# Kernel optimization log

Hardware: AMD Instinct MI355X
Metric: run time of the kernel (lower is better)

The kernel has to match this reference:

```python
import jax, jax.numpy as jnp
import numpy as np

B, S, D = 1, 512, 2048
H, KVH, HD = 16, 16, 128          # heads, kv heads, head_dim = D // H
E, K, I = 64, 6, 1408             # routed experts, top_k, moe intermediate
NSH = 2
ISH = NSH * I                     # shared expert intermediate
EPS = 1e-6
THETA = 10000.0
SCALE = HD ** -0.5


def setup_inputs() -> dict:
    key = jax.random.key(0)
    ks = jax.random.split(key, 12)
    s = 0.02
    rn = lambda k, shape: s * jax.random.normal(k, shape, dtype=jnp.float32)
    return {
        "positions": jnp.arange(B * S, dtype=jnp.int32).reshape(B, S),
        "hidden_states": jax.random.normal(ks[0], (B, S, D), dtype=jnp.float32),
        "residual": jax.random.normal(ks[1], (B, S, D), dtype=jnp.float32),
        "ln1_w": jnp.ones((D,), jnp.float32),
        "ln2_w": jnp.ones((D,), jnp.float32),
        "wqkv": rn(ks[2], ((H + 2 * KVH) * HD, D)),
        "wo": rn(ks[3], (D, H * HD)),
        "gate_w": rn(ks[4], (E, D)),
        "w1": rn(ks[5], (E, 2 * I, D)),   # packed gate_up per expert
        "w2": rn(ks[6], (E, D, I)),       # down per expert
        "sw1": rn(ks[7], (2 * ISH, D)),   # shared expert gate_up
        "sw2": rn(ks[8], (D, ISH)),       # shared expert down
    }


def _rmsnorm(x, w):
    var = jnp.mean(x * x, axis=-1, keepdims=True)
    return x * jax.lax.rsqrt(var + EPS) * w


def _rope(x, pos):
    # x: [B, S, n_heads, HD], neox style (rotate halves), full rotary dim
    half = HD // 2
    inv_freq = 1.0 / (THETA ** (jnp.arange(half, dtype=jnp.float32) * 2.0 / HD))
    ang = pos.astype(jnp.float32)[..., None] * inv_freq        # [B, S, half]
    cos = jnp.cos(ang)[:, :, None, :]
    sin = jnp.sin(ang)[:, :, None, :]
    x1, x2 = jnp.split(x, 2, axis=-1)
    return jnp.concatenate([x1 * cos - x2 * sin, x2 * cos + x1 * sin], axis=-1)


def _swiglu(x, w_gate_up, w_down):
    gu = x @ w_gate_up.T
    g, u = jnp.split(gu, 2, axis=-1)
    return (jax.nn.silu(g) * u) @ w_down.T


def reference(positions, hidden_states, residual, ln1_w, ln2_w, wqkv, wo,
              gate_w, w1, w2, sw1, sw2):
    # --- input_layernorm with fused residual add (vLLM RMSNorm semantics) ---
    x = hidden_states + residual
    residual = x
    h = _rmsnorm(x, ln1_w)

    # --- attention: qkv proj, RoPE, causal attention (prefill), o proj ---
    qkv = h @ wqkv.T                                           # [B, S, (H+2KVH)*HD]
    q, k, v = jnp.split(qkv, [H * HD, (H + KVH) * HD], axis=-1)
    q = q.reshape(B, S, H, HD)
    k = k.reshape(B, S, KVH, HD)
    v = v.reshape(B, S, KVH, HD)
    q = _rope(q, positions)
    k = _rope(k, positions)
    scores = jnp.einsum("bqhd,bkhd->bhqk", q, k) * SCALE
    causal = jnp.tril(jnp.ones((S, S), dtype=bool))
    scores = jnp.where(causal, scores, -jnp.inf)
    attn = jax.nn.softmax(scores, axis=-1)
    ctx = jnp.einsum("bhqk,bkhd->bqhd", attn, v).reshape(B, S, H * HD)
    h = ctx @ wo.T

    # --- post_attention_layernorm with fused residual add ---
    x = h + residual
    residual = x
    h = _rmsnorm(x, ln2_w)

    # --- MoE: shared expert + softmax gate + top-k dispatch ---
    xt = h.reshape(B * S, D)                                   # [T, D]
    T = B * S
    shared = _swiglu(xt, sw1, sw2)                             # [T, D]
    logits = xt @ gate_w.T                                     # [T, E]
    probs = jax.nn.softmax(logits.astype(jnp.float32), axis=-1)
    topw, topi = jax.lax.top_k(probs, K)                       # [T, K]
    # norm_topk_prob = False -> no renormalization
    combine = jnp.zeros((T, E), jnp.float32).at[
        jnp.arange(T)[:, None], topi].add(topw)                # [T, E]

    def expert_step(acc, ew):
        w1e, w2e, ce = ew                                      # [2I,D], [D,I], [T]
        out = _swiglu(xt, w1e, w2e)                            # [T, D]
        return acc + ce[:, None] * out, None

    moe_out, _ = jax.lax.scan(expert_step, jnp.zeros_like(xt),
                              (w1, w2, combine.T))
    out = (moe_out + shared).reshape(B, S, D)
    return out, residual
```

## Files before the change

### kernel.cpp

```cpp
#include <hip/hip_runtime.h>
#include <hip/hip_bf16.h>


typedef __attribute__((ext_vector_type(4))) float  f32x4;
typedef __attribute__((ext_vector_type(8))) short  short8;
typedef __attribute__((ext_vector_type(8))) unsigned short ushort8;

#define SS    512
#define DD    2048
#define NH    16
#define HDIM  128
#define NQKV  6144
#define NEXP  64
#define TOPK  6
#define IEXP  1408
#define ISHE  2816
#define MAXTILE 128
#define ATT_SCALE 0.08838834764831845f

__device__ __forceinline__ float u2f(unsigned short u) {
  return __uint_as_float(((unsigned int)u) << 16);
}
__device__ __forceinline__ unsigned short f2u(float f) {
  __hip_bfloat16 h = __float2bfloat16(f);
  return *reinterpret_cast<unsigned short*>(&h);
}
__device__ __forceinline__ ushort8 cvt8(f32x4 a, f32x4 b) {
  ushort8 r;
  r[0]=f2u(a[0]); r[1]=f2u(a[1]); r[2]=f2u(a[2]); r[3]=f2u(a[3]);
  r[4]=f2u(b[0]); r[5]=f2u(b[1]); r[6]=f2u(b[2]); r[7]=f2u(b[3]);
  return r;
}

typedef __attribute__((address_space(3))) unsigned int lds_uint;
typedef const __attribute__((address_space(1))) unsigned int ga_uint;
__device__ __forceinline__ void gll16(const void* g, void* l) {
  __builtin_amdgcn_global_load_lds((ga_uint*)g, (lds_uint*)l, 16, 0, 0);
}

__global__ __launch_bounds__(256) void cvtw_k(
    const float* __restrict__ wqkv, const float* __restrict__ wo,
    const float* __restrict__ sw1, const float* __restrict__ sw2,
    unsigned short* __restrict__ wqkv_bf, unsigned short* __restrict__ wo_bf,
    unsigned short* __restrict__ sw1_bf, unsigned short* __restrict__ sw2_bf)
{
  long long i = ((long long)blockIdx.x * 256 + threadIdx.x) * 8;
  const long long S1 = (long long)NQKV * DD;
  const long long S2 = S1 + (long long)DD * DD;
  const long long S3 = S2 + (long long)2 * ISHE * DD;
  const float* src; unsigned short* dst; long long j;
  if (i < S1)      { src = wqkv; dst = wqkv_bf; j = i; }
  else if (i < S2) { src = wo;   dst = wo_bf;   j = i - S1; }
  else if (i < S3) { src = sw1;  dst = sw1_bf;  j = i - S2; }
  else             { src = sw2;  dst = sw2_bf;  j = i - S3; }
  f32x4 a = *(const f32x4*)(src + j);
  f32x4 b = *(const f32x4*)(src + j + 4);
  *(ushort8*)(dst + j) = cvt8(a, b);
}

__global__ __launch_bounds__(256) void addnorm1_k(
    const float* __restrict__ hid, const float* __restrict__ res,
    const float* __restrict__ w, float* __restrict__ x1,
    unsigned short* __restrict__ h1)
{
  int t = blockIdx.x, tid = threadIdx.x;
  long long base = (long long)t * DD + tid * 8;
  float x[8]; float ss = 0.f;
#pragma unroll
  for (int i = 0; i < 8; i++) {
    x[i] = hid[base + i] + res[base + i];
    ss += x[i] * x[i]; x1[base + i] = x[i];
  }
#pragma unroll
  for (int o = 1; o < 64; o <<= 1) ss += __shfl_xor(ss, o);
  __shared__ float r4[4];
  if ((tid & 63) == 0) r4[tid >> 6] = ss;
  __syncthreads();
  ss = r4[0] + r4[1] + r4[2] + r4[3];
  float rr = rsqrtf(ss * (1.f / DD) + 1e-6f);
#pragma unroll
  for (int i = 0; i < 8; i++) h1[base + i] = f2u(x[i] * rr * w[tid * 8 + i]);
}

__global__ __launch_bounds__(256) void addnorm2_k(
    const unsigned short* __restrict__ attn, const float* __restrict__ x1,
    const float* __restrict__ w, float* __restrict__ resid_out,
    unsigned short* __restrict__ h3)
{
  int t = blockIdx.x, tid = threadIdx.x;
  long long base = (long long)t * DD + tid * 8;
  ushort8 va = *(const ushort8*)(attn + base);
  float x[8]; float ss = 0.f;
#pragma unroll
  for (int i = 0; i < 8; i++) {
    x[i] = u2f(va[i]) + x1[base + i]; ss += x[i] * x[i];
    resid_out[base + i] = x[i];
  }
#pragma unroll
  for (int o = 1; o < 64; o <<= 1) ss += __shfl_xor(ss, o);
  __shared__ float r4[4];
  if ((tid & 63) == 0) r4[tid >> 6] = ss;
  __syncthreads();
  ss = r4[0] + r4[1] + r4[2] + r4[3];
  float rr = rsqrtf(ss * (1.f / DD) + 1e-6f);
#pragma unroll
  for (int i = 0; i < 8; i++) h3[base + i] = f2u(x[i] * rr * w[tid * 8 + i]);
}

__global__ __launch_bounds__(256) void gemm_bb(
    const unsigned short* __restrict__ A, const unsigned short* __restrict__ W,
    unsigned short* __restrict__ C, int Nh, int K, int lda)
{
  __shared__ __align__(16) unsigned short As[2][64][64];
  __shared__ __align__(16) unsigned short Bs[2][64][64];

  int m0 = blockIdx.y * 64;
  int n0 = blockIdx.x * 64;
  int tid = threadIdx.x, lane = tid & 63, w = tid >> 6;

  const unsigned short* asrc[2];
  const unsigned short* bsrc[2];
#pragma unroll
  for (int i = 0; i < 2; i++) {
    int c = w + i * 4;
    int r = c * 8 + (lane >> 3);
    int col = ((lane & 7) ^ (lane >> 3)) << 3;
    asrc[i] = A + (long long)(m0 + r) * lda + col;
    bsrc[i] = W + (long long)(n0 + r) * K + col;
  }

  int wm = (w >> 1) * 32, wn = (w & 1) * 32;
  int l15 = lane & 15, hi = lane >> 4;
  int key = l15 & 7;

  f32x4 acc[2][2] = {};

#define BSTAGE(buf, k0)                                                  \
  do {                                                                   \
    gll16((const char*)asrc[0] + (k0) * 2, &As[buf][w * 8][0]);          \
    gll16((const char*)asrc[1] + (k0) * 2, &As[buf][(w + 4) * 8][0]);    \
    gll16((const char*)bsrc[0] + (k0) * 2, &Bs[buf][w * 8][0]);          \
    gll16((const char*)bsrc[1] + (k0) * 2, &Bs[buf][(w + 4) * 8][0]);    \
  } while (0)

  BSTAGE(0, 0);
  int buf = 0;
  for (int k0 = 0; k0 < K; k0 += 64, buf ^= 1) {
    __syncthreads();
    if (k0 + 64 < K) BSTAGE(buf ^ 1, k0 + 64);
#pragma unroll
    for (int kk = 0; kk < 2; kk++) {
      short8 fa[2], fb[2];
#pragma unroll
      for (int f = 0; f < 2; f++) {
        fa[f] = *(const short8*)&As[buf][wm + f * 16 + l15][(((kk << 2) + hi) ^ key) << 3];
        fb[f] = *(const short8*)&Bs[buf][wn + f * 16 + l15][(((kk << 2) + hi) ^ key) << 3];
      }
#pragma unroll
      for (int fm = 0; fm < 2; fm++)
#pragma unroll
        for (int fn = 0; fn < 2; fn++)
          acc[fm][fn] = __builtin_amdgcn_mfma_f32_16x16x32_bf16(fa[fm], fb[fn], acc[fm][fn], 0, 0, 0);
    }
  }
#undef BSTAGE

  int r0q = hi * 4;
#pragma unroll
  for (int fm = 0; fm < 2; fm++) {
#pragma unroll
    for (int j = 0; j < 4; j++) {
      int m = m0 + wm + fm * 16 + r0q + j;
      unsigned short* Cp = C + (long long)m * Nh + n0 + wn;
#pragma unroll
      for (int fn = 0; fn < 2; fn++)
        Cp[fn * 16 + l15] = f2u(acc[fm][fn][j]);
    }
  }
}

template<int STAGE>
__global__ __launch_bounds__(256) void moe_k(
    const unsigned short* __restrict__ h3,
    const unsigned short* __restrict__ act_e_in, const unsigned short* __restrict__ act_sh_in,
    const float* __restrict__ w1, const unsigned short* __restrict__ sw1_bf,
    const float* __restrict__ w2, const unsigned short* __restrict__ sw2_bf,
    unsigned short* __restrict__ act_e_out, unsigned short* __restrict__ act_sh_out,
    unsigned short* __restrict__ out_e, unsigned short* __restrict__ shared_o,
    const int* __restrict__ e_cnt, const int* __restrict__ e_off,
    const int* __restrict__ tok_list, const float* __restrict__ wslot,
    const int* __restrict__ tile_tab, const int* __restrict__ ntiles)
{
  constexpr bool SILU = (STAGE == 0);
  __shared__ __align__(16) unsigned short As[64][72];
  __shared__ __align__(16) unsigned short Bg[64][72];
  __shared__ __align__(16) unsigned short Bu[SILU ? 64 : 1][72];

  int yr = blockIdx.y;
  int y = (yr < 8) ? yr : 8 + ((yr - 8) & 7) * 15 + ((yr - 8) >> 3);
  if (y >= *ntiles) return;
  int tt = tile_tab[y];
  int e = tt >> 8;
  int m0 = (tt & 255) * 64;
  bool sh = (e == NEXP);
  int cnt  = sh ? SS : e_cnt[e];
  int roff = sh ? 0 : e_off[e];
  int n0 = blockIdx.x * 64;

  int Nh, K, lda;
  const float* Wb32 = nullptr;
  const unsigned short* Wb16 = nullptr;
  const unsigned short* Abase;
  unsigned short* Cb;
  if (STAGE == 0) {
    K = DD; lda = DD; Abase = h3;
    if (sh) { Nh = ISHE; Wb16 = sw1_bf; Cb = act_sh_out; }
    else    { Nh = IEXP; Wb32 = w1 + (long long)e * 2 * IEXP * DD; Cb = act_e_out; }
    if (n0 >= Nh) return;
  } else {
    Nh = DD;
    if (sh) { K = ISHE; lda = ISHE; Abase = act_sh_in; Wb16 = sw2_bf; Cb = shared_o; }
    else    { K = IEXP; lda = IEXP; Abase = act_e_in;
              Wb32 = w2 + (long long)e * DD * IEXP; Cb = out_e; }
  }

  int tid = threadIdx.x;
  int sr  = tid >> 2;
  int sce = (tid & 3) * 16;

  int am = m0 + sr; if (am >= cnt) am = cnt - 1;
  int arow;
  if (STAGE == 0) arow = sh ? am : tok_list[roff + am];
  else            arow = sh ? am : roff + am;
  const unsigned short* ap = Abase + (long long)arow * lda + sce;
  const float*          gp32 = Wb32 ? (Wb32 + (long long)(n0 + sr) * K + sce) : nullptr;
  const float*          up32 = (Wb32 && SILU) ? (Wb32 + (long long)(Nh + n0 + sr) * K + sce) : nullptr;
  const unsigned short* gp16 = Wb16 ? (Wb16 + (long long)(n0 + sr) * K + sce) : nullptr;
  const unsigned short* up16 = (Wb16 && SILU) ? (Wb16 + (long long)(Nh + n0 + sr) * K + sce) : nullptr;

  int lane = tid & 63, wid = tid >> 6;
  int wm = (wid >> 1) * 32, wn = (wid & 1) * 32;
  int l15 = lane & 15, hi = lane >> 4;

  f32x4 acc[2][2] = {};
  f32x4 accU[2][2] = {};
  ushort8 raA0, raA1, raB0, raB1;
  f32x4 rgA[4], ruA[4], rgB[4], ruB[4];
  union BC { f32x4 f; ushort8 s; };

#define MLOAD(k, r0, r1, g, u)                                     \
  do {                                                             \
    r0 = *(const ushort8*)(ap + (k));                              \
    r1 = *(const ushort8*)(ap + (k) + 8);                          \
    if (sh) {                                                      \
      g[0] = *(const f32x4*)(gp16 + (k));                          \
      g[1] = *(const f32x4*)(gp16 + (k) + 8);                      \
      if (SILU) {                                                  \
        u[0] = *(const f32x4*)(up16 + (k));                        \
        u[1] = *(const f32x4*)(up16 + (k) + 8);                    \
      }                                                            \
    } else {                                                       \
      _Pragma("unroll")                                            \
      for (int i_ = 0; i_ < 4; i_++) g[i_] = *(const f32x4*)(gp32 + (k) + 4 * i_); \
      if (SILU) {                                                  \
        _Pragma("unroll")                                          \
        for (int i_ = 0; i_ < 4; i_++) u[i_] = *(const f32x4*)(up32 + (k) + 4 * i_); \
      }                                                            \
    }                                                              \
  } while (0)

#define MSTORE(r0, r1, g, u)                                       \
  do {                                                             \
    *(ushort8*)&As[sr][sce]     = r0;                              \
    *(ushort8*)&As[sr][sce + 8] = r1;                              \
    if (sh) {                                                      \
      BC b0, b1; b0.f = g[0]; b1.f = g[1];                         \
      *(ushort8*)&Bg[sr][sce]     = b0.s;                          \
      *(ushort8*)&Bg[sr][sce + 8] = b1.s;                          \
      if (SILU) {                                                  \
        BC c0, c1; c0.f = u[0]; c1.f = u[1];                       \
        *(ushort8*)&Bu[sr][sce]     = c0.s;                        \
        *(ushort8*)&Bu[sr][sce + 8] = c1.s;                        \
      }                                                            \
    } else {                                                       \
      *(ushort8*)&Bg[sr][sce]     = cvt8(g[0], g[1]);              \
      *(ushort8*)&Bg[sr][sce + 8] = cvt8(g[2], g[3]);              \
      if (SILU) {                                                  \
        *(ushort8*)&Bu[sr][sce]     = cvt8(u[0], u[1]);            \
        *(ushort8*)&Bu[sr][sce + 8] = cvt8(u[2], u[3]);            \
      }                                                            \
    }                                                              \
  } while (0)

#define MMFMA                                                      \
  do {                                                             \
    _Pragma("unroll")                                              \
    for (int kk = 0; kk < 2; kk++) {                               \
      int kc = kk * 32 + hi * 8;                                   \
      short8 fa[2], fg[2];                                         \
      _Pragma("unroll")                                            \
      for (int f = 0; f < 2; f++) {                                \
        fa[f] = *(const short8*)&As[wm + f * 16 + l15][kc];        \
        fg[f] = *(const short8*)&Bg[wn + f * 16 + l15][kc];        \
      }                                                            \
      _Pragma("unroll")                                            \
      for (int fm = 0; fm < 2; fm++)                               \
        _Pragma("unroll")                                          \
        for (int fn = 0; fn < 2; fn++)                             \
          acc[fm][fn] = __builtin_amdgcn_mfma_f32_16x16x32_bf16(fa[fm], fg[fn], acc[fm][fn], 0, 0, 0); \
      if (SILU) {                                                  \
        short8 fu[2];                                              \
        _Pragma("unroll")                                          \
        for (int f = 0; f < 2; f++) fu[f] = *(const short8*)&Bu[wn + f * 16 + l15][kc]; \
        _Pragma("unroll")                                          \
        for (int fm = 0; fm < 2; fm++)                             \
          _Pragma("unroll")                                        \
          for (int fn = 0; fn < 2; fn++)                           \
            accU[fm][fn] = __builtin_amdgcn_mfma_f32_16x16x32_bf16(fa[fm], fu[fn], accU[fm][fn], 0, 0, 0); \
      }                                                            \
    }                                                              \
  } while (0)

  MLOAD(0,  raA0, raA1, rgA, ruA);
  MLOAD(64, raB0, raB1, rgB, ruB);
  for (int k0 = 0; k0 < K; k0 += 128) {
    __syncthreads();
    MSTORE(raA0, raA1, rgA, ruA);
    __syncthreads();
    if (k0 + 128 < K) MLOAD(k0 + 128, raA0, raA1, rgA, ruA);
    MMFMA;
    __syncthreads();
    MSTORE(raB0, raB1, rgB, ruB);
    __syncthreads();
    if (k0 + 192 < K) MLOAD(k0 + 192, raB0, raB1, rgB, ruB);
    MMFMA;
  }
#undef MLOAD
#undef MSTORE
#undef MMFMA

  int r0q = hi * 4;
#pragma unroll
  for (int fm = 0; fm < 2; fm++) {
#pragma unroll
    for (int j = 0; j < 4; j++) {
      int m = m0 + wm + fm * 16 + r0q + j;
      if (m >= cnt) continue;
      long long crow = sh ? m : (roff + m);
      float scale = (STAGE == 1 && !sh) ? wslot[crow] : 1.f;
      unsigned short* Cp = Cb + crow * (long long)Nh + n0 + wn;
#pragma unroll
      for (int fn = 0; fn < 2; fn++) {
        float v;
        if (SILU) {
          float g = acc[fm][fn][j], u = accU[fm][fn][j];
          v = (g / (1.f + __expf(-g))) * u;
        } else v = acc[fm][fn][j];
        Cp[fn * 16 + l15] = f2u(v * scale);
      }
    }
  }
}

__global__ __launch_bounds__(256) void rope_k(
    const int* __restrict__ pos, const unsigned short* __restrict__ qkv,
    unsigned short* __restrict__ qr, unsigned short* __restrict__ kr)
{
  int t = blockIdx.x, tid = threadIdx.x;
  __shared__ float cs[64], sn[64];
  if (tid < 64) {
    float inv = __expf(-((float)(2 * tid) / 128.f) * logf(10000.f));
    float ang = (float)pos[t] * inv;
    cs[tid] = cosf(ang); sn[tid] = sinf(ang);
  }
  __syncthreads();
  const unsigned short* row = qkv + (long long)t * NQKV;
  for (int idx = tid; idx < NH * 64; idx += 256) {
    int hh = idx >> 6, i = idx & 63;
    long long o = ((long long)hh * SS + t) * HDIM;
    float x1 = u2f(row[hh*128 + i]), x2 = u2f(row[hh*128 + i + 64]);
    qr[o + i]      = f2u(x1 * cs[i] - x2 * sn[i]);
    qr[o + i + 64] = f2u(x2 * cs[i] + x1 * sn[i]);
    float y1 = u2f(row[2048 + hh*128 + i]), y2 = u2f(row[2048 + hh*128 + i + 64]);
    kr[o + i]      = f2u(y1 * cs[i] - y2 * sn[i]);
    kr[o + i + 64] = f2u(y2 * cs[i] + y1 * sn[i]);
  }
}

__global__ __launch_bounds__(128) void attn_k(
    const unsigned short* __restrict__ qr, const unsigned short* __restrict__ kr,
    const unsigned short* __restrict__ qkv, unsigned short* __restrict__ ctx)
{
  int h = blockIdx.x, qt = blockIdx.y, q0 = qt * 32;
  int tid = threadIdx.x, lane = tid & 63, w = tid >> 6;
  int l15 = lane & 15, hi = lane >> 4;

  __shared__ unsigned short Vt[128][72];
  __shared__ unsigned short Pl[2][16][72];

  short8 qf[4];
  const unsigned short* Qb = qr + ((long long)h * SS + q0 + w * 16 + l15) * HDIM + hi * 8;
#pragma unroll
  for (int kf = 0; kf < 4; kf++) qf[kf] = *(const short8*)(Qb + kf * 32);

  f32x4 o[8] = {};
  float m_run[4] = {-1e30f, -1e30f, -1e30f, -1e30f};
  float l_run[4] = {};
  int myq = w * 16 + hi * 4;

  int T = (q0 + 31) >> 6;
  int qoff = q0 - 64 * T;
  for (int kt = 0; kt <= T; kt++) {
    int kbase = kt * 64;
    __syncthreads();
    {
      int r = lane, d0 = w * 64;
      const unsigned short* Vp = qkv + (long long)(kbase + r) * NQKV + 4096 + h * HDIM + d0;
#pragma unroll
      for (int c = 0; c < 8; c++) {
        ushort8 v = *(const ushort8*)(Vp + c * 8);
#pragma unroll
        for (int i = 0; i < 8; i++) Vt[d0 + c * 8 + i][r] = v[i];
      }
    }
    f32x4 s[4] = {};
    const unsigned short* Kb = kr + ((long long)h * SS + kbase) * HDIM + hi * 8;
#pragma unroll
    for (int nf = 0; nf < 4; nf++) {
      const unsigned short* Kp = Kb + (long long)(nf * 16 + l15) * HDIM;
#pragma unroll
      for (int kf = 0; kf < 4; kf++) {
        short8 kf8 = *(const short8*)(Kp + kf * 32);
        s[nf] = __builtin_amdgcn_mfma_f32_16x16x32_bf16(qf[kf], kf8, s[nf], 0, 0, 0);
      }
    }
    bool last = (kt == T);
#pragma unroll
    for (int nf = 0; nf < 4; nf++) {
      int keyl = nf * 16 + l15;
#pragma unroll
      for (int j = 0; j < 4; j++) {
        float sv = s[nf][j] * ATT_SCALE;
        if (last && keyl > qoff + myq + j) sv = -1e30f;
        s[nf][j] = sv;
      }
    }
    float corr[4], mnew[4];
#pragma unroll
    for (int j = 0; j < 4; j++) {
      float mv = fmaxf(fmaxf(s[0][j], s[1][j]), fmaxf(s[2][j], s[3][j]));
#pragma unroll
      for (int ox = 1; ox < 16; ox <<= 1) mv = fmaxf(mv, __shfl_xor(mv, ox));
      mnew[j] = fmaxf(m_run[j], mv);
      corr[j] = __expf(m_run[j] - mnew[j]);
      m_run[j] = mnew[j];
    }
#pragma unroll
    for (int nf8 = 0; nf8 < 8; nf8++)
#pragma unroll
      for (int j = 0; j < 4; j++) o[nf8][j] *= corr[j];
    float rs[4] = {};
#pragma unroll
    for (int nf = 0; nf < 4; nf++) {
#pragma unroll
      for (int j = 0; j < 4; j++) {
        float pv = __expf(s[nf][j] - mnew[j]);
        rs[j] += pv;
        Pl[w][hi * 4 + j][nf * 16 + l15] = f2u(pv);
      }
    }
#pragma unroll
    for (int j = 0; j < 4; j++) {
      float sv = rs[j];
#pragma unroll
      for (int ox = 1; ox < 16; ox <<= 1) sv += __shfl_xor(sv, ox);
      l_run[j] = l_run[j] * corr[j] + sv;
    }
    __syncthreads();
#pragma unroll
    for (int kf2 = 0; kf2 < 2; kf2++) {
      short8 pa = *(const short8*)&Pl[w][l15][kf2 * 32 + hi * 8];
#pragma unroll
      for (int nf8 = 0; nf8 < 8; nf8++) {
        short8 vb = *(const short8*)&Vt[nf8 * 16 + l15][kf2 * 32 + hi * 8];
        o[nf8] = __builtin_amdgcn_mfma_f32_16x16x32_bf16(pa, vb, o[nf8], 0, 0, 0);
      }
    }
  }
#pragma unroll
  for (int j = 0; j < 4; j++) {
    float inv = 1.f / l_run[j];
    long long t = q0 + myq + j;
    unsigned short* Cp = ctx + t * (long long)DD + h * HDIM;
#pragma unroll
    for (int nf8 = 0; nf8 < 8; nf8++)
      Cp[nf8 * 16 + l15] = f2u(o[nf8][j] * inv);
  }
}

__global__ __launch_bounds__(256) void gating_k(
    const unsigned short* __restrict__ h3, const float* __restrict__ gw,
    int* __restrict__ topi, float* __restrict__ topw)
{
  int b = blockIdx.x, tid = threadIdx.x;
  int e = tid & 63, g = tid >> 6;
  __shared__ float p[8][NEXP];
  const float* wr = gw + (long long)e * DD;
  int t0 = b * 8 + g * 2;
  const unsigned short* h0 = h3 + (long long)t0 * DD;
  const unsigned short* h1 = h0 + DD;
  float a0 = 0.f, a1 = 0.f;
  for (int k = 0; k < DD; k += 8) {
    f32x4 w0 = *(const f32x4*)(wr + k);
    f32x4 w1 = *(const f32x4*)(wr + k + 4);
    ushort8 x0 = *(const ushort8*)(h0 + k);
    ushort8 x1 = *(const ushort8*)(h1 + k);
    a0 += u2f(x0[0])*w0[0] + u2f(x0[1])*w0[1] + u2f(x0[2])*w0[2] + u2f(x0[3])*w0[3]
        + u2f(x0[4])*w1[0] + u2f(x0[5])*w1[1] + u2f(x0[6])*w1[2] + u2f(x0[7])*w1[3];
    a1 += u2f(x1[0])*w0[0] + u2f(x1[1])*w0[1] + u2f(x1[2])*w0[2] + u2f(x1[3])*w0[3]
        + u2f(x1[4])*w1[0] + u2f(x1[5])*w1[1] + u2f(x1[6])*w1[2] + u2f(x1[7])*w1[3];
  }
  p[g * 2][e] = a0; p[g * 2 + 1][e] = a1;
  __syncthreads();
  if (tid < 8) {
    int t = b * 8 + tid;
    float* pr = p[tid];
    float mx = -1e30f;
    for (int j = 0; j < NEXP; j++) mx = fmaxf(mx, pr[j]);
    float s = 0.f;
    for (int j = 0; j < NEXP; j++) { pr[j] = __expf(pr[j] - mx); s += pr[j]; }
    float invs = 1.f / s;
    for (int j = 0; j < NEXP; j++) pr[j] *= invs;
    for (int r = 0; r < TOPK; r++) {
      int bi = 0; float bv = -1.f;
      for (int j = 0; j < NEXP; j++) if (pr[j] > bv) { bv = pr[j]; bi = j; }
      topi[t * TOPK + r] = bi; topw[t * TOPK + r] = bv; pr[bi] = -2.f;
    }
  }
}

__global__ __launch_bounds__(256) void route_k(
    const int* __restrict__ topi, const float* __restrict__ topw,
    int* __restrict__ ecnt, int* __restrict__ eoff,
    int* __restrict__ tok_list, int* __restrict__ slotg,
    float* __restrict__ wslot, int* __restrict__ tile_tab,
    int* __restrict__ ntiles)
{
  __shared__ int ti[SS * TOPK];
  __shared__ int c4[NEXP][4];
  __shared__ int ctot[NEXP];
  __shared__ int offs[NEXP + 1];
  int tid = threadIdx.x;
  for (int i = tid; i < SS * TOPK; i += 256) ti[i] = topi[i];
  __syncthreads();
  int e = tid >> 2, q = tid & 3;
  const int QW = SS * TOPK / 4;
  int lo = q * QW, hiQ = lo + QW;
  int n = 0;
  for (int i = lo; i < hiQ; i++) n += (ti[i] == e);
  c4[e][q] = n;
  __syncthreads();
  if (q == 0) {
    int s = c4[e][0] + c4[e][1] + c4[e][2] + c4[e][3];
    ctot[e] = s; ecnt[e] = s;
  }
  __syncthreads();
  if (tid == 0) {
    offs[0] = 0;
    for (int k = 0; k < NEXP; k++) offs[k + 1] = offs[k] + ctot[k];
    int nt = 0;
    for (int mt = 0; mt < SS / 64; mt++) tile_tab[nt++] = (NEXP << 8) | mt;
    for (int k = 0; k < NEXP; k++)
      for (int mt = 0; mt * 64 < ctot[k]; mt++) tile_tab[nt++] = (k << 8) | mt;
    *ntiles = nt;
  }
  __syncthreads();
  if (q == 0) eoff[e] = offs[e];
  int idx = offs[e];
  for (int qq = 0; qq < q; qq++) idx += c4[e][qq];
  for (int i = lo; i < hiQ; i++)
    if (ti[i] == e) {
      tok_list[idx] = i / TOPK; slotg[i] = idx; wslot[idx] = topw[i]; idx++;
    }
}

__global__ __launch_bounds__(256) void combine_k(
    const unsigned short* __restrict__ shared_o, const unsigned short* __restrict__ out_e,
    const int* __restrict__ slotg, float* __restrict__ outp)
{
  int t = blockIdx.x, tid = threadIdx.x;
  int sl[TOPK];
#pragma unroll
  for (int j = 0; j < TOPK; j++) sl[j] = slotg[t * TOPK + j];
  long long d0 = (long long)t * DD + tid * 8;
  ushort8 sh = *(const ushort8*)(shared_o + d0);
  float a[8];
#pragma unroll
  for (int i = 0; i < 8; i++) a[i] = u2f(sh[i]);
#pragma unroll
  for (int j = 0; j < TOPK; j++) {
    ushort8 v = *(const ushort8*)(out_e + (long long)sl[j] * DD + tid * 8);
#pragma unroll
    for (int i = 0; i < 8; i++) a[i] += u2f(v[i]);
  }
#pragma unroll
  for (int i = 0; i < 8; i++) outp[d0 + i] = a[i];
}

extern "C" void kernel_launch(void* const* d_in, const int* in_sizes, int n_in,
                              void* d_out, int out_size, void* d_ws, size_t ws_size,
                              hipStream_t stream)
{
  (void)in_sizes; (void)n_in; (void)out_size; (void)ws_size;
  const int*   positions = (const int*)d_in[0];
  const float* hidden    = (const float*)d_in[1];
  const float* residual  = (const float*)d_in[2];
  const float* ln1_w     = (const float*)d_in[3];
  const float* ln2_w     = (const float*)d_in[4];
  const float* wqkv      = (const float*)d_in[5];
  const float* wo        = (const float*)d_in[6];
  const float* gate_w    = (const float*)d_in[7];
  const float* w1        = (const float*)d_in[8];
  const float* w2        = (const float*)d_in[9];
  const float* sw1       = (const float*)d_in[10];
  const float* sw2       = (const float*)d_in[11];

  float* outp      = (float*)d_out;
  float* resid_out = outp + (size_t)SS * DD;

  char* p = (char*)d_ws;
  auto alloc = [&](size_t b) { void* r = p; p += (b + 255) & ~(size_t)255; return r; };
  float*          x1       = (float*)alloc((size_t)SS * DD * 4);
  unsigned short* h1       = (unsigned short*)alloc((size_t)SS * DD * 2);
  unsigned short* qkv      = (unsigned short*)alloc((size_t)SS * NQKV * 2);
  unsigned short* qr       = (unsigned short*)alloc((size_t)SS * DD * 2);
  unsigned short* kr       = (unsigned short*)alloc((size_t)SS * DD * 2);
  unsigned short* ctx      = (unsigned short*)alloc((size_t)SS * DD * 2);
  unsigned short* attnout  = (unsigned short*)alloc((size_t)SS * DD * 2);
  unsigned short* h3       = (unsigned short*)alloc((size_t)SS * DD * 2);
  unsigned short* act_sh   = (unsigned short*)alloc((size_t)SS * ISHE * 2);
  unsigned short* shared_o = (unsigned short*)alloc((size_t)SS * DD * 2);
  unsigned short* act_e    = (unsigned short*)alloc((size_t)SS * TOPK * IEXP * 2);
  unsigned short* out_e    = (unsigned short*)alloc((size_t)SS * TOPK * DD * 2);
  unsigned short* wqkv_bf  = (unsigned short*)alloc((size_t)NQKV * DD * 2);
  unsigned short* wo_bf    = (unsigned short*)alloc((size_t)DD * DD * 2);
  unsigned short* sw1_bf   = (unsigned short*)alloc((size_t)2 * ISHE * DD * 2);
  unsigned short* sw2_bf   = (unsigned short*)alloc((size_t)DD * ISHE * 2);
  int*            topi     = (int*)alloc(SS * TOPK * 4);
  float*          topw     = (float*)alloc(SS * TOPK * 4);
  int*            slotg    = (int*)alloc(SS * TOPK * 4);
  int*            tok_list = (int*)alloc(SS * TOPK * 4);
  float*          wslot    = (float*)alloc(SS * TOPK * 4);
  int*            ecnt     = (int*)alloc(NEXP * 4);
  int*            eoff     = (int*)alloc(NEXP * 4);
  int*            tile_tab = (int*)alloc(MAXTILE * 4);
  int*            ntiles   = (int*)alloc(4);

  const long long CVT_ELEMS = (long long)NQKV * DD + (long long)DD * DD
                            + (long long)2 * ISHE * DD + (long long)DD * ISHE;
  cvtw_k<<<(unsigned)(CVT_ELEMS / 2048), 256, 0, stream>>>(
      wqkv, wo, sw1, sw2, wqkv_bf, wo_bf, sw1_bf, sw2_bf);
  addnorm1_k<<<SS, 256, 0, stream>>>(hidden, residual, ln1_w, x1, h1);
  gemm_bb<<<dim3(NQKV/64, SS/64), 256, 0, stream>>>(h1, wqkv_bf, qkv, NQKV, DD, DD);
  rope_k<<<SS, 256, 0, stream>>>(positions, qkv, qr, kr);
  attn_k<<<dim3(NH, SS/32), 128, 0, stream>>>(qr, kr, qkv, ctx);
  gemm_bb<<<dim3(DD/64, SS/64), 256, 0, stream>>>(ctx, wo_bf, attnout, DD, DD, DD);
  addnorm2_k<<<SS, 256, 0, stream>>>(attnout, x1, ln2_w, resid_out, h3);
  gating_k<<<SS/8, 256, 0, stream>>>(h3, gate_w, topi, topw);
  route_k<<<1, 256, 0, stream>>>(topi, topw, ecnt, eoff, tok_list, slotg, wslot,
                                 tile_tab, ntiles);
  moe_k<0><<<dim3(ISHE/64, MAXTILE), 256, 0, stream>>>(
      h3, nullptr, nullptr, w1, sw1_bf, w2, sw2_bf, act_e, act_sh, nullptr, nullptr,
      ecnt, eoff, tok_list, wslot, tile_tab, ntiles);
  moe_k<1><<<dim3(DD/64, MAXTILE), 256, 0, stream>>>(
      nullptr, act_e, act_sh, w1, sw1_bf, w2, sw2_bf, nullptr, nullptr, out_e, shared_o,
      ecnt, eoff, tok_list, wslot, tile_tab, ntiles);
  combine_k<<<SS, 256, 0, stream>>>(shared_o, out_e, slotg, outp);
}
```

Baseline: 810.7 us.

## Fuse add-norm with gating and split shared-expert MoE tiles to trim idle blocks

Merges the second residual-add RMSNorm with the router gating kernel, so each block normalizes 8 tokens into LDS and computes gate logits and top-k from there, removing one launch and a reread of h3. The MoE stage-0 grid shrinks from ISHE/64 to IEXP/64 columns. The shared expert's gate_up work is split into two half-width tile entries so no blocks exit early on the n0 >= Nh check, and separate tile tables are built for each stage. The fused kernel runs on only 64 blocks with serialized per-token normalization, which may reduce parallelism for that phase.

```diff
diff --git a/kernel.cpp b/kernel.cpp
--- a/kernel.cpp
+++ b/kernel.cpp
@@ -15,7 +15,8 @@
 #define TOPK  6
 #define IEXP  1408
 #define ISHE  2816
-#define MAXTILE 128
+#define NT0   128
+#define NT1   120
 #define ATT_SCALE 0.08838834764831845f
 
 __device__ __forceinline__ float u2f(unsigned short u) {
@@ -82,29 +83,73 @@
   for (int i = 0; i < 8; i++) h1[base + i] = f2u(x[i] * rr * w[tid * 8 + i]);
 }
 
-__global__ __launch_bounds__(256) void addnorm2_k(
+__global__ __launch_bounds__(256) void an2gate_k(
     const unsigned short* __restrict__ attn, const float* __restrict__ x1,
     const float* __restrict__ w, float* __restrict__ resid_out,
-    unsigned short* __restrict__ h3)
-{
-  int t = blockIdx.x, tid = threadIdx.x;
-  long long base = (long long)t * DD + tid * 8;
-  ushort8 va = *(const ushort8*)(attn + base);
-  float x[8]; float ss = 0.f;
-#pragma unroll
-  for (int i = 0; i < 8; i++) {
-    x[i] = u2f(va[i]) + x1[base + i]; ss += x[i] * x[i];
-    resid_out[base + i] = x[i];
-  }
-#pragma unroll
-  for (int o = 1; o < 64; o <<= 1) ss += __shfl_xor(ss, o);
+    unsigned short* __restrict__ h3, const float* __restrict__ gw,
+    int* __restrict__ topi, float* __restrict__ topw)
+{
+  __shared__ unsigned short hs[8][DD];
   __shared__ float r4[4];
-  if ((tid & 63) == 0) r4[tid >> 6] = ss;
+  __shared__ float p[8][NEXP];
+  int b = blockIdx.x, tid = threadIdx.x;
+
+  for (int tk = 0; tk < 8; tk++) {
+    int t = b * 8 + tk;
+    long long base = (long long)t * DD + tid * 8;
+    ushort8 va = *(const ushort8*)(attn + base);
+    float x[8]; float ss = 0.f;
+#pragma unroll
+    for (int i = 0; i < 8; i++) {
+      x[i] = u2f(va[i]) + x1[base + i]; ss += x[i] * x[i];
+      resid_out[base + i] = x[i];
+    }
+#pragma unroll
+    for (int o = 1; o < 64; o <<= 1) ss += __shfl_xor(ss, o);
+    if ((tid & 63) == 0) r4[tid >> 6] = ss;
+    __syncthreads();
+    ss = r4[0] + r4[1] + r4[2] + r4[3];
+    float rr = rsqrtf(ss * (1.f / DD) + 1e-6f);
+    ushort8 hv;
+#pragma unroll
+    for (int i = 0; i < 8; i++) hv[i] = f2u(x[i] * rr * w[tid * 8 + i]);
+    *(ushort8*)&hs[tk][tid * 8] = hv;
+    *(ushort8*)(h3 + base) = hv;
+    __syncthreads();
+  }
+
+  int e = tid & 63, g = tid >> 6;
+  const float* wr = gw + (long long)e * DD;
+  const unsigned short* h0 = hs[g * 2];
+  const unsigned short* h1r = hs[g * 2 + 1];
+  float a0 = 0.f, a1 = 0.f;
+  for (int k = 0; k < DD; k += 8) {
+    f32x4 w0 = *(const f32x4*)(wr + k);
+    f32x4 w1 = *(const f32x4*)(wr + k + 4);
+    ushort8 x0 = *(const ushort8*)(h0 + k);
+    ushort8 x1v = *(const ushort8*)(h1r + k);
+    a0 += u2f(x0[0])*w0[0] + u2f(x0[1])*w0[1] + u2f(x0[2])*w0[2] + u2f(x0[3])*w0[3]
+        + u2f(x0[4])*w1[0] + u2f(x0[5])*w1[1] + u2f(x0[6])*w1[2] + u2f(x0[7])*w1[3];
+    a1 += u2f(x1v[0])*w0[0] + u2f(x1v[1])*w0[1] + u2f(x1v[2])*w0[2] + u2f(x1v[3])*w0[3]
+        + u2f(x1v[4])*w1[0] + u2f(x1v[5])*w1[1] + u2f(x1v[6])*w1[2] + u2f(x1v[7])*w1[3];
+  }
+  p[g * 2][e] = a0; p[g * 2 + 1][e] = a1;
   __syncthreads();
-  ss = r4[0] + r4[1] + r4[2] + r4[3];
-  float rr = rsqrtf(ss * (1.f / DD) + 1e-6f);
-#pragma unroll
-  for (int i = 0; i < 8; i++) h3[base + i] = f2u(x[i] * rr * w[tid * 8 + i]);
+  if (tid < 8) {
+    int t = b * 8 + tid;
+    float* pr = p[tid];
+    float mx = -1e30f;
+    for (int j = 0; j < NEXP; j++) mx = fmaxf(mx, pr[j]);
+    float s = 0.f;
+    for (int j = 0; j < NEXP; j++) { pr[j] = __expf(pr[j] - mx); s += pr[j]; }
+    float invs = 1.f / s;
+    for (int j = 0; j < NEXP; j++) pr[j] *= invs;
+    for (int r = 0; r < TOPK; r++) {
+      int bi = 0; float bv = -1.f;
+      for (int j = 0; j < NEXP; j++) if (pr[j] > bv) { bv = pr[j]; bi = j; }
+      topi[t * TOPK + r] = bi; topw[t * TOPK + r] = bv; pr[bi] = -2.f;
+    }
+  }
 }
 
 __global__ __launch_bounds__(256) void gemm_bb(
@@ -197,15 +242,18 @@
   __shared__ __align__(16) unsigned short Bu[SILU ? 64 : 1][72];
 
   int yr = blockIdx.y;
-  int y = (yr < 8) ? yr : 8 + ((yr - 8) & 7) * 15 + ((yr - 8) >> 3);
+  int y;
+  if (STAGE == 0) y = (yr < 16) ? yr : 16 + ((yr - 16) & 7) * 14 + ((yr - 16) >> 3);
+  else            y = (yr < 8)  ? yr : 8  + ((yr - 8) & 7) * 14 + ((yr - 8) >> 3);
   if (y >= *ntiles) return;
   int tt = tile_tab[y];
-  int e = tt >> 8;
+  int e = tt >> 16;
+  int half = (tt >> 8) & 1;
   int m0 = (tt & 255) * 64;
   bool sh = (e == NEXP);
   int cnt  = sh ? SS : e_cnt[e];
   int roff = sh ? 0 : e_off[e];
-  int n0 = blockIdx.x * 64;
+  int n0 = blockIdx.x * 64 + ((STAGE == 0 && sh) ? half * IEXP : 0);
 
   int Nh, K, lda;
   const float* Wb32 = nullptr;
@@ -216,7 +264,6 @@
     K = DD; lda = DD; Abase = h3;
     if (sh) { Nh = ISHE; Wb16 = sw1_bf; Cb = act_sh_out; }
     else    { Nh = IEXP; Wb32 = w1 + (long long)e * 2 * IEXP * DD; Cb = act_e_out; }
-    if (n0 >= Nh) return;
   } else {
     Nh = DD;
     if (sh) { K = ISHE; lda = ISHE; Abase = act_sh_in; Wb16 = sw2_bf; Cb = shared_o; }
@@ -498,53 +545,13 @@
   }
 }
 
-__global__ __launch_bounds__(256) void gating_k(
-    const unsigned short* __restrict__ h3, const float* __restrict__ gw,
-    int* __restrict__ topi, float* __restrict__ topw)
-{
-  int b = blockIdx.x, tid = threadIdx.x;
-  int e = tid & 63, g = tid >> 6;
-  __shared__ float p[8][NEXP];
-  const float* wr = gw + (long long)e * DD;
-  int t0 = b * 8 + g * 2;
-  const unsigned short* h0 = h3 + (long long)t0 * DD;
-  const unsigned short* h1 = h0 + DD;
-  float a0 = 0.f, a1 = 0.f;
-  for (int k = 0; k < DD; k += 8) {
-    f32x4 w0 = *(const f32x4*)(wr + k);
-    f32x4 w1 = *(const f32x4*)(wr + k + 4);
-    ushort8 x0 = *(const ushort8*)(h0 + k);
-    ushort8 x1 = *(const ushort8*)(h1 + k);
-    a0 += u2f(x0[0])*w0[0] + u2f(x0[1])*w0[1] + u2f(x0[2])*w0[2] + u2f(x0[3])*w0[3]
-        + u2f(x0[4])*w1[0] + u2f(x0[5])*w1[1] + u2f(x0[6])*w1[2] + u2f(x0[7])*w1[3];
-    a1 += u2f(x1[0])*w0[0] + u2f(x1[1])*w0[1] + u2f(x1[2])*w0[2] + u2f(x1[3])*w0[3]
-        + u2f(x1[4])*w1[0] + u2f(x1[5])*w1[1] + u2f(x1[6])*w1[2] + u2f(x1[7])*w1[3];
-  }
-  p[g * 2][e] = a0; p[g * 2 + 1][e] = a1;
-  __syncthreads();
-  if (tid < 8) {
-    int t = b * 8 + tid;
-    float* pr = p[tid];
-    float mx = -1e30f;
-    for (int j = 0; j < NEXP; j++) mx = fmaxf(mx, pr[j]);
-    float s = 0.f;
-    for (int j = 0; j < NEXP; j++) { pr[j] = __expf(pr[j] - mx); s += pr[j]; }
-    float invs = 1.f / s;
-    for (int j = 0; j < NEXP; j++) pr[j] *= invs;
-    for (int r = 0; r < TOPK; r++) {
-      int bi = 0; float bv = -1.f;
-      for (int j = 0; j < NEXP; j++) if (pr[j] > bv) { bv = pr[j]; bi = j; }
-      topi[t * TOPK + r] = bi; topw[t * TOPK + r] = bv; pr[bi] = -2.f;
-    }
-  }
-}
-
 __global__ __launch_bounds__(256) void route_k(
     const int* __restrict__ topi, const float* __restrict__ topw,
     int* __restrict__ ecnt, int* __restrict__ eoff,
     int* __restrict__ tok_list, int* __restrict__ slotg,
-    float* __restrict__ wslot, int* __restrict__ tile_tab,
-    int* __restrict__ ntiles)
+    float* __restrict__ wslot, int* __restrict__ tile_tab0,
+    int* __restrict__ tile_tab1, int* __restrict__ ntiles0,
+    int* __restrict__ ntiles1)
 {
   __shared__ int ti[SS * TOPK];
   __shared__ int c4[NEXP][4];
@@ -568,11 +575,18 @@
   if (tid == 0) {
     offs[0] = 0;
     for (int k = 0; k < NEXP; k++) offs[k + 1] = offs[k] + ctot[k];
-    int nt = 0;
-    for (int mt = 0; mt < SS / 64; mt++) tile_tab[nt++] = (NEXP << 8) | mt;
+    int n0 = 0, n1 = 0;
+    for (int mt = 0; mt < SS / 64; mt++) {
+      tile_tab0[n0++] = (NEXP << 16) | (0 << 8) | mt;
+      tile_tab0[n0++] = (NEXP << 16) | (1 << 8) | mt;
+      tile_tab1[n1++] = (NEXP << 16) | mt;
+    }
     for (int k = 0; k < NEXP; k++)
-      for (int mt = 0; mt * 64 < ctot[k]; mt++) tile_tab[nt++] = (k << 8) | mt;
-    *ntiles = nt;
+      for (int mt = 0; mt * 64 < ctot[k]; mt++) {
+        tile_tab0[n0++] = (k << 16) | mt;
+        tile_tab1[n1++] = (k << 16) | mt;
+      }
+    *ntiles0 = n0; *ntiles1 = n1;
   }
   __syncthreads();
   if (q == 0) eoff[e] = offs[e];
@@ -653,8 +667,10 @@
   float*          wslot    = (float*)alloc(SS * TOPK * 4);
   int*            ecnt     = (int*)alloc(NEXP * 4);
   int*            eoff     = (int*)alloc(NEXP * 4);
-  int*            tile_tab = (int*)alloc(MAXTILE * 4);
-  int*            ntiles   = (int*)alloc(4);
+  int*            tile_tab0= (int*)alloc(NT0 * 4);
+  int*            tile_tab1= (int*)alloc(NT1 * 4);
+  int*            ntiles0  = (int*)alloc(4);
+  int*            ntiles1  = (int*)alloc(4);
 
   const long long CVT_ELEMS = (long long)NQKV * DD + (long long)DD * DD
                             + (long long)2 * ISHE * DD + (long long)DD * ISHE;
@@ -665,15 +681,15 @@
   rope_k<<<SS, 256, 0, stream>>>(positions, qkv, qr, kr);
   attn_k<<<dim3(NH, SS/32), 128, 0, stream>>>(qr, kr, qkv, ctx);
   gemm_bb<<<dim3(DD/64, SS/64), 256, 0, stream>>>(ctx, wo_bf, attnout, DD, DD, DD);
-  addnorm2_k<<<SS, 256, 0, stream>>>(attnout, x1, ln2_w, resid_out, h3);
-  gating_k<<<SS/8, 256, 0, stream>>>(h3, gate_w, topi, topw);
+  an2gate_k<<<SS/8, 256, 0, stream>>>(attnout, x1, ln2_w, resid_out, h3,
+                                      gate_w, topi, topw);
   route_k<<<1, 256, 0, stream>>>(topi, topw, ecnt, eoff, tok_list, slotg, wslot,
-                                 tile_tab, ntiles);
-  moe_k<0><<<dim3(ISHE/64, MAXTILE), 256, 0, stream>>>(
+                                 tile_tab0, tile_tab1, ntiles0, ntiles1);
+  moe_k<0><<<dim3(IEXP/64, NT0), 256, 0, stream>>>(
       h3, nullptr, nullptr, w1, sw1_bf, w2, sw2_bf, act_e, act_sh, nullptr, nullptr,
-      ecnt, eoff, tok_list, wslot, tile_tab, ntiles);
-  moe_k<1><<<dim3(DD/64, MAXTILE), 256, 0, stream>>>(
+      ecnt, eoff, tok_list, wslot, tile_tab0, ntiles0);
+  moe_k<1><<<dim3(DD/64, NT1), 256, 0, stream>>>(
       nullptr, act_e, act_sh, w1, sw1_bf, w2, sw2_bf, nullptr, nullptr, out_e, shared_o,
-      ecnt, eoff, tok_list, wslot, tile_tab, ntiles);
+      ecnt, eoff, tok_list, wslot, tile_tab1, ntiles1);
   combine_k<<<SS, 256, 0, stream>>>(shared_o, out_e, slotg, outp);
 }
```

After: 764.0 us. -5.8%, faster.
